# Performance work log

Measured on AMD Instinct MI355X. Metric: run time of the kernel, lower is better.

The kernel has to match this reference:

```python
import jax, jax.numpy as jnp
import numpy as np

N, E, IN, OUT, ED, NT, H = 20000, 640000, 128, 256, 32, 16, 8
GATC = OUT // 2          # 128 per-layer GAT width
C = GATC // H            # 16 per-head dim
GINEC = OUT - GATC       # 128


def setup_inputs() -> dict:
    key = jax.random.key(0)
    ks = jax.random.split(key, 16)
    s = 0.05
    return {
        "x": jax.random.normal(ks[0], (N, IN), jnp.float32),
        "edge_index": jax.random.randint(ks[1], (2, E), 0, N, jnp.int64),
        "edge_attr": jax.random.normal(ks[2], (E, ED), jnp.float32),
        "edge_types": jax.random.randint(ks[3], (E,), 0, NT, jnp.int64),
        "gat_W": jax.random.normal(ks[4], (IN, H * C), jnp.float32) * s,
        "gat_b": jnp.zeros((H * C,), jnp.float32),
        "gat_edge_W": jax.random.normal(ks[5], (ED, H * C), jnp.float32) * s,
        "gat_a_src": jax.random.normal(ks[6], (H, C), jnp.float32) * s,
        "gat_a_dst": jax.random.normal(ks[7], (H, C), jnp.float32) * s,
        "gat_a_edge": jax.random.normal(ks[8], (H, C), jnp.float32) * s,
        "gat_type_emb": jax.random.normal(ks[9], (NT, ED), jnp.float32) * s,
        "gine_type_emb": jax.random.normal(ks[10], (NT, ED), jnp.float32) * s,
        "gine_edge_W": jax.random.normal(ks[11], (ED, IN), jnp.float32) * s,
        "gine_edge_b": jnp.zeros((IN,), jnp.float32),
        "gine_eps": jnp.zeros((1,), jnp.float32),
        "gine_W1": jax.random.normal(ks[12], (IN, GINEC), jnp.float32) * s,
        "gine_b1": jnp.zeros((GINEC,), jnp.float32),
        "gine_W2": jax.random.normal(ks[13], (GINEC, GINEC), jnp.float32) * s,
        "gine_b2": jnp.zeros((GINEC,), jnp.float32),
        "comb_W": jax.random.normal(ks[14], (H * C + GINEC, OUT), jnp.float32) * s,
        "comb_b": jnp.zeros((OUT,), jnp.float32),
        "ln_g": jnp.ones((OUT,), jnp.float32),
        "ln_b": jnp.zeros((OUT,), jnp.float32),
    }


def reference(x, edge_index, edge_attr, edge_types,
              gat_W, gat_b, gat_edge_W, gat_a_src, gat_a_dst, gat_a_edge,
              gat_type_emb, gine_type_emb, gine_edge_W, gine_edge_b, gine_eps,
              gine_W1, gine_b1, gine_W2, gine_b2, comb_W, comb_b, ln_g, ln_b):
    n = x.shape[0]
    h_, c_ = gat_a_src.shape
    src, dst = edge_index[0], edge_index[1]

    # ---- GAT branch (edge-featured multi-head attention) ----
    e = edge_attr + gat_type_emb[edge_types]                      # [E, ED]
    h = (x @ gat_W).reshape(n, h_, c_)                            # [N, H, C]
    ee = (e @ gat_edge_W).reshape(-1, h_, c_)                     # [E, H, C]
    a_s = jnp.einsum('nhc,hc->nh', h, gat_a_src)                  # [N, H]
    a_d = jnp.einsum('nhc,hc->nh', h, gat_a_dst)
    a_e = jnp.einsum('ehc,hc->eh', ee, gat_a_edge)                # [E, H]
    logit = jax.nn.leaky_relu(a_s[src] + a_d[dst] + a_e, 0.2)     # [E, H]
    # segment softmax over incoming edges of each destination node
    mx = jax.ops.segment_max(logit, dst, num_segments=n)
    p = jnp.exp(logit - mx[dst])
    denom = jax.ops.segment_sum(p, dst, num_segments=n)
    alpha = p / (denom[dst] + 1e-16)                              # [E, H]
    msg = alpha[:, :, None] * h[src]                              # [E, H, C]
    gat_out = jax.ops.segment_sum(msg, dst, num_segments=n).reshape(n, h_ * c_) + gat_b

    # ---- GINE branch ----
    ep = (edge_attr + gine_type_emb[edge_types]) @ gine_edge_W + gine_edge_b  # [E, IN]
    agg = jax.ops.segment_sum(jax.nn.relu(x[src] + ep), dst, num_segments=n)
    h2 = (1.0 + gine_eps[0]) * x + agg
    gine_out = jax.nn.relu(h2 @ gine_W1 + gine_b1) @ gine_W2 + gine_b2        # [N, GINEC]

    # ---- fuse: Linear + LayerNorm + ReLU (dropout is identity in eval) ----
    z = jnp.concatenate([gat_out, gine_out], axis=-1) @ comb_W + comb_b       # [N, OUT]
    mu = jnp.mean(z, axis=-1, keepdims=True)
    var = jnp.var(z, axis=-1, keepdims=True)
    z = (z - mu) * jax.lax.rsqrt(var + 1e-5) * ln_g + ln_b
    return jax.nn.relu(z)
```

## Files before the change

### kernel.cpp

```cpp
#include <hip/hip_runtime.h>

#define N_NODES 20000
#define N_EDGES 640000

typedef _Float16 h2v   __attribute__((ext_vector_type(2)));
typedef _Float16 h16x8 __attribute__((ext_vector_type(8)));
typedef float    f32x4v __attribute__((ext_vector_type(4)));
typedef unsigned u32x4v __attribute__((ext_vector_type(4)));

__device__ __forceinline__ unsigned packh2(float a, float b){
    h2v v; v.x = (_Float16)a; v.y = (_Float16)b;
    return __builtin_bit_cast(unsigned, v);
}

__global__ void k0_zero(float4* __restrict__ p, int n4){
    int i = blockIdx.x*blockDim.x + threadIdx.x;
    int stride = gridDim.x*blockDim.x;
    float4 z; z.x=0.f; z.y=0.f; z.z=0.f; z.w=0.f;
    for (; i<n4; i+=stride) p[i] = z;
}

__global__ void kD_detect(const int* __restrict__ eidx_w, const int* __restrict__ ety_w,
                          int* __restrict__ flags){
    int i = blockIdx.x*blockDim.x + threadIdx.x;
    int stride = gridDim.x*blockDim.x;
    int a0 = 0, a1 = 0;
    for (int w = 2*i+1; w < 2*N_EDGES; w += 2*stride) a0 |= eidx_w[w];
    for (int w = 2*i+1; w < N_EDGES;   w += 2*stride) a1 |= ety_w[w];
    if (a0) atomicOr(&flags[0], 1);
    if (a1) atomicOr(&flags[1], 1);
}

__global__ void kN_norm(const int* __restrict__ eidx_w, const int* __restrict__ ety_w,
                        const int* __restrict__ flags,
                        int* __restrict__ dst, int* __restrict__ srcty,
                        int* __restrict__ cnt){
    int i = blockIdx.x*blockDim.x + threadIdx.x;
    int stride = gridDim.x*blockDim.x;
    const bool e32 = (flags[0] != 0);
    const bool t32 = (flags[1] != 0);
    for (int e = i; e < N_EDGES; e += stride){
        int s, d, t;
        if (e32){ s = eidx_w[e];   d = eidx_w[N_EDGES + e]; }
        else    { s = eidx_w[2*e]; d = eidx_w[2*N_EDGES + 2*e]; }
        t = t32 ? ety_w[e] : ety_w[2*e];
        s = min(max(s, 0), N_NODES-1);
        d = min(max(d, 0), N_NODES-1);
        t = min(max(t, 0), 15);
        dst[e] = d; srcty[e] = s | (t << 20);
        atomicAdd(&cnt[d], 1);
    }
}

__global__ __launch_bounds__(1024) void kS_scan(const int* __restrict__ cnt,
                                                int* __restrict__ row_ptr,
                                                int* __restrict__ cursor){
    __shared__ int sW[16];
    __shared__ int sWS[16];
    __shared__ int sbase;
    const int t = threadIdx.x, lane = t & 63, wv = t >> 6;
    if (t==0) sbase = 0;
    __syncthreads();
    for (int base=0; base<N_NODES; base+=4096){
        const int idx0 = base + t*4;
        int v0 = (idx0  <N_NODES) ? cnt[idx0  ] : 0;
        int v1 = (idx0+1<N_NODES) ? cnt[idx0+1] : 0;
        int v2 = (idx0+2<N_NODES) ? cnt[idx0+2] : 0;
        int v3 = (idx0+3<N_NODES) ? cnt[idx0+3] : 0;
        int p1 = v0+v1, p2 = p1+v2, tot = p2+v3;
        int xs = tot;
        #pragma unroll
        for (int off=1; off<64; off<<=1){
            int y = __shfl_up(xs, off, 64);
            if (lane >= off) xs += y;
        }
        if (lane==63) sW[wv] = xs;
        __syncthreads();
        if (t < 16){
            int wvv = sW[t], ws = wvv;
            #pragma unroll
            for (int off=1; off<16; off<<=1){
                int y = __shfl_up(ws, off, 16);
                if ((t&15) >= off) ws += y;
            }
            sWS[t] = ws - wvv;
        }
        __syncthreads();
        int ex = sbase + sWS[wv] + xs - tot;
        if (idx0  <N_NODES){ row_ptr[idx0  ]=ex;    cursor[idx0  ]=ex;    }
        if (idx0+1<N_NODES){ row_ptr[idx0+1]=ex+v0; cursor[idx0+1]=ex+v0; }
        if (idx0+2<N_NODES){ row_ptr[idx0+2]=ex+p1; cursor[idx0+2]=ex+p1; }
        if (idx0+3<N_NODES){ row_ptr[idx0+3]=ex+p2; cursor[idx0+3]=ex+p2; }
        __syncthreads();
        if (t==0) sbase += sWS[15] + sW[15];
        __syncthreads();
    }
    if (t==0) row_ptr[N_NODES] = sbase;
}

__global__ __launch_bounds__(256) void kPre(const float* __restrict__ gat_edge_W,
                                            const float* __restrict__ a_edge,
                                            const float* __restrict__ gat_emb,
                                            const float* __restrict__ gine_emb,
                                            const float* __restrict__ gine_edge_W,
                                            const float* __restrict__ gine_edge_b,
                                            float* __restrict__ Mt, float* __restrict__ ATw,
                                            float* __restrict__ Tw){
    const int t = threadIdx.x;
    if (blockIdx.x < 16){
        if (t < 128){
            const int tyv = blockIdx.x;
            float acc = gine_edge_b[t];
            #pragma unroll
            for (int d=0;d<32;d++) acc += gine_emb[tyv*32+d]*gine_edge_W[d*128+t];
            Tw[tyv*128+t] = acc;
        }
        return;
    }
    __shared__ float sM[32*8];
    const int d = t>>3, hh = t&7;
    float acc = 0.f;
    #pragma unroll
    for (int c=0;c<16;c++) acc += gat_edge_W[d*128 + hh*16 + c]*a_edge[hh*16 + c];
    sM[d*8+hh] = acc; Mt[hh*32 + d] = acc;
    __syncthreads();
    if (t < 128){
        int tyv = t>>3, h2 = t&7;
        float a = 0.f;
        #pragma unroll
        for (int dd=0;dd<32;dd++) a += gat_emb[tyv*32+dd]*sM[dd*8+h2];
        ATw[tyv*8+h2] = a;
    }
}

__global__ __launch_bounds__(128) void k1_node_prep(
    const float* __restrict__ x, const float* __restrict__ gat_W,
    const float* __restrict__ a_src, const float* __restrict__ a_dst,
    unsigned* __restrict__ xhb, float* __restrict__ as_out, float* __restrict__ ad_out)
{
    __shared__ float sX[8][128];
    __shared__ float sH[128];
    const int t = threadIdx.x;
    const int base = blockIdx.x*8;
    const float4* xin = (const float4*)(x + (size_t)base*128);
    float4* sx4 = (float4*)&sX[0][0];
    for (int i=t;i<256;i+=128) sx4[i] = xin[i];
    __syncthreads();
    float acc[8] = {0,0,0,0,0,0,0,0};
    for (int k=0;k<128;k++){
        float w = gat_W[k*128 + t];
        #pragma unroll
        for (int nn=0;nn<8;nn++) acc[nn] += sX[nn][k]*w;
    }
    const float asv = a_src[t], advv = a_dst[t];
    #pragma unroll
    for (int nn=0;nn<8;nn++){
        const int n = base + nn;
        float vs = acc[nn]*asv, vd = acc[nn]*advv;
        #pragma unroll
        for (int off=8; off>=1; off>>=1){ vs += __shfl_xor(vs,off,16); vd += __shfl_xor(vd,off,16); }
        if ((t&15)==0){ as_out[n*8 + (t>>4)] = vs; ad_out[n*8 + (t>>4)] = vd; }
        __syncthreads();
        sH[t] = acc[nn];
        __syncthreads();
        if (t < 64){
            xhb[(size_t)n*128 + t] = packh2(sX[nn][2*t], sX[nn][2*t+1]);
        } else {
            int i = t - 64;
            xhb[(size_t)n*128 + 64 + i] = packh2(sH[2*i], sH[2*i+1]);
        }
    }
}

__global__ __launch_bounds__(256) void kCE_edge(
    const float* __restrict__ eattr,
    const int* __restrict__ dstA, const int* __restrict__ styA,
    const float* __restrict__ a_s, const float* __restrict__ a_d,
    const float* __restrict__ Mt, const float* __restrict__ ATw,
    const float* __restrict__ gine_emb,
    int* __restrict__ cursor,
    unsigned* __restrict__ evb, float* __restrict__ p_s, int* __restrict__ sty_s)
{
    __shared__ float sEv[32][36];
    __shared__ float sMt[8][36];
    __shared__ float sAT[16*8];
    __shared__ int sPos[32];
    const int t = threadIdx.x;
    sMt[t>>5][t&31] = Mt[t];
    if (t < 128) sAT[t] = ATw[t];
    const int et = t>>3, q = t&7;
    for (int base = blockIdx.x*32; base < N_EDGES; base += gridDim.x*32){
        __syncthreads();
        const int e = base + et;
        float4 f = ((const float4*)eattr)[(size_t)e*8 + q];
        *(float4*)&sEv[et][q*4] = f;
        const int d = dstA[e];
        const int sty = styA[e];
        if (q==0) sPos[et] = atomicAdd(&cursor[d], 1);
        __syncthreads();
        const int pos = sPos[et];
        const int srcn = sty & 0xFFFFF;
        const int tyv = ((unsigned)sty)>>20;
        const float4 ge = ((const float4*)gine_emb)[tyv*8 + q];
        ((uint2*)evb)[(size_t)pos*8 + q] =
            make_uint2(packh2(f.x+ge.x, f.y+ge.y), packh2(f.z+ge.z, f.w+ge.w));
        float acc = 0.f;
        #pragma unroll
        for (int m=0;m<8;m++){
            float4 ev4 = *(const float4*)&sEv[et][m*4];
            float4 m4  = *(const float4*)&sMt[q][m*4];
            acc += ev4.x*m4.x + ev4.y*m4.y + ev4.z*m4.z + ev4.w*m4.w;
        }
        float lg = a_s[srcn*8+q] + a_d[d*8+q] + acc + sAT[tyv*8+q];
        lg = (lg>0.f) ? lg : 0.2f*lg;
        p_s[(size_t)pos*8 + q] = __expf(lg);
        if (q==0) sty_s[pos] = sty;
    }
}

template<bool MASK>
__device__ __forceinline__ void gine_block16(
    int pos0, int rem, int m, int g,
    const unsigned* __restrict__ xhb, const unsigned* __restrict__ evb,
    const float* __restrict__ p_s, const int* __restrict__ sty_s,
    const h16x8* aw, const float* bb,
    float* accA, float* accG, float* ps)
{
    const int mc = MASK ? (m < rem ? m : rem - 1) : m;
    u32x4v uu = ((const u32x4v*)evb)[(size_t)(pos0 + mc)*4 + g];
    h16x8 evf = __builtin_bit_cast(h16x8, uu);

    const _Float16* xp[4];
    int ecl[4];
    #pragma unroll
    for (int r=0;r<4;r++){
        const int er = 4*g + r;
        const int ec = MASK ? (er < rem ? er : rem - 1) : er;
        ecl[r] = pos0 + ec;
        const int srcn = sty_s[pos0 + ec] & 0xFFFFF;
        xp[r] = (const _Float16*)(xhb + (size_t)srcn*128) + m;
    }
    #pragma unroll
    for (int hf4=0; hf4<2; hf4++){
        f32x4v pv[4];
        #pragma unroll
        for (int r=0;r<4;r++){
            pv[r] = *(const f32x4v*)(p_s + (size_t)ecl[r]*8 + hf4*4);
            if (MASK && (4*g + r) >= rem) pv[r] = (f32x4v){0.f,0.f,0.f,0.f};
        }
        #pragma unroll
        for (int r=0;r<4;r++){
            ps[hf4*4+0] += pv[r][0]; ps[hf4*4+1] += pv[r][1];
            ps[hf4*4+2] += pv[r][2]; ps[hf4*4+3] += pv[r][3];
        }
        #pragma unroll
        for (int cc=0; cc<4; cc++){
            const int c = hf4*4 + cc;
            f32x4v Dv = { bb[c], bb[c], bb[c], bb[c] };
            Dv = __builtin_amdgcn_mfma_f32_16x16x32_f16(evf, aw[c], Dv, 0, 0, 0);
            #pragma unroll
            for (int r=0;r<4;r++){
                float xf = (float)xp[r][c*16];
                float hf = (float)xp[r][128 + c*16];
                float tmp = fmaxf(xf + Dv[r], 0.f);
                if (MASK && (4*g + r) >= rem) tmp = 0.f;
                accA[c] += tmp;
                accG[c] += pv[r][cc] * hf;
            }
        }
    }
}

__global__ __launch_bounds__(256) void k3_gather(
    const unsigned* __restrict__ xhb, const unsigned* __restrict__ evb,
    const float* __restrict__ p_s, const int* __restrict__ sty_s,
    const int* __restrict__ row_ptr,
    const float* __restrict__ gine_b, const float* __restrict__ gine_W,
    float* __restrict__ agg, float* __restrict__ gacc)
{
    const int t = threadIdx.x;
    const int lane = t & 63;
    const int m = lane & 15;
    const int g = lane >> 4;

    h16x8 aw[8];
    #pragma unroll
    for (int c=0;c<8;c++){
        #pragma unroll
        for (int j=0;j<8;j++)
            aw[c][j] = (_Float16)gine_W[(8*g + j)*128 + c*16 + m];
    }
    float bb[8];
    #pragma unroll
    for (int c=0;c<8;c++) bb[c] = gine_b[c*16 + m];

    const int nwaves = gridDim.x*4;
    for (int d = blockIdx.x*4 + (t>>6); d < N_NODES; d += nwaves){
        const int row = row_ptr[d], end = row_ptr[d+1];
        float accA[8] = {0,0,0,0,0,0,0,0};
        float accG[8] = {0,0,0,0,0,0,0,0};
        float ps[8]   = {0,0,0,0,0,0,0,0};
        const int deg = end - row;
        int pos0 = row;
        const int nfull = deg >> 4;
        for (int b=0;b<nfull;b++, pos0+=16)
            gine_block16<false>(pos0, 16, m, g, xhb, evb, p_s, sty_s, aw, bb, accA, accG, ps);
        const int rem = deg & 15;
        if (rem)
            gine_block16<true>(pos0, rem, m, g, xhb, evb, p_s, sty_s, aw, bb, accA, accG, ps);
        #pragma unroll
        for (int c=0;c<8;c++){
            accA[c] += __shfl_xor(accA[c], 16, 64);
            accA[c] += __shfl_xor(accA[c], 32, 64);
            accG[c] += __shfl_xor(accG[c], 16, 64);
            accG[c] += __shfl_xor(accG[c], 32, 64);
            ps[c]   += __shfl_xor(ps[c],   16, 64);
            ps[c]   += __shfl_xor(ps[c],   32, 64);
        }
        if (g == 0){
            #pragma unroll
            for (int c=0;c<8;c++){
                const float inv = 1.f/(ps[c] + 1e-16f);
                agg [(size_t)d*128 + c*16 + m] = accA[c];
                gacc[(size_t)d*128 + c*16 + m] = accG[c]*inv;
            }
        }
    }
}

#define NPB 8
__global__ __launch_bounds__(256) void k4_final(
    const float* __restrict__ x, const float* __restrict__ agg, const float* __restrict__ gat_acc,
    const float* __restrict__ gat_b, const float* __restrict__ eps_p,
    const float* __restrict__ W1, const float* __restrict__ b1,
    const float* __restrict__ W2, const float* __restrict__ gb2,
    const float* __restrict__ comb_W, const float* __restrict__ comb_b,
    const float* __restrict__ ln_g, const float* __restrict__ ln_b,
    float* __restrict__ out)
{
    __shared__ float sZt[256][NPB];
    __shared__ float sH2[2][128][4];
    __shared__ float sT1[2][128][4];
    __shared__ float sP1[4], sP2[4];
    __shared__ float sMu, sRs;
    const int t = threadIdx.x;
    const int half = t >> 7;
    const int j = t & 127;
    const float epsv = 1.f + eps_p[0];

    {
        float hq[4];
        #pragma unroll
        for (int q=0;q<4;q++){
            const int nn = half*4 + q;
            const int n = blockIdx.x*NPB + nn;
            hq[q] = epsv*x[(size_t)n*128 + j] + agg[(size_t)n*128 + j];
            sZt[j][nn] = gat_acc[(size_t)n*128 + j] + gat_b[j];
        }
        *(float4*)&sH2[half][j][0] = make_float4(hq[0],hq[1],hq[2],hq[3]);
    }
    __syncthreads();
    {
        float acc[4];
        const float b1j = b1[j];
        #pragma unroll
        for (int q=0;q<4;q++) acc[q] = b1j;
        for (int k=0;k<128;k++){
            float w = W1[k*128 + j];
            float4 hv = *(const float4*)&sH2[half][k][0];
            acc[0] += hv.x*w; acc[1] += hv.y*w; acc[2] += hv.z*w; acc[3] += hv.w*w;
        }
        *(float4*)&sT1[half][j][0] = make_float4(fmaxf(acc[0],0.f), fmaxf(acc[1],0.f),
                                                 fmaxf(acc[2],0.f), fmaxf(acc[3],0.f));
    }
    __syncthreads();
    {
        float acc[4];
        const float b2j = gb2[j];
        #pragma unroll
        for (int q=0;q<4;q++) acc[q] = b2j;
        for (int k=0;k<128;k++){
            float w = W2[k*128 + j];
            float4 tv = *(const float4*)&sT1[half][k][0];
            acc[0] += tv.x*w; acc[1] += tv.y*w; acc[2] += tv.z*w; acc[3] += tv.w*w;
        }
        #pragma unroll
        for (int q=0;q<4;q++) sZt[128 + j][half*4 + q] = acc[q];
    }
    __syncthreads();

    float z[NPB];
    const float cb = comb_b[t];
    #pragma unroll
    for (int nn=0;nn<NPB;nn++) z[nn] = cb;
    for (int k=0;k<256;k++){
        float w = comb_W[k*256 + t];
        float4 a = *(const float4*)&sZt[k][0];
        float4 b = *(const float4*)&sZt[k][4];
        z[0] += a.x*w; z[1] += a.y*w; z[2] += a.z*w; z[3] += a.w*w;
        z[4] += b.x*w; z[5] += b.y*w; z[6] += b.z*w; z[7] += b.w*w;
    }

    const float g  = ln_g[t];
    const float bb = ln_b[t];
    for (int nn=0;nn<NPB;nn++){
        const int n = blockIdx.x*NPB + nn;
        float zv = z[nn];
        float s1 = zv, s2 = zv*zv;
        #pragma unroll
        for (int off=32; off>=1; off>>=1){ s1 += __shfl_xor(s1,off,64); s2 += __shfl_xor(s2,off,64); }
        if ((t&63)==0){ sP1[t>>6]=s1; sP2[t>>6]=s2; }
        __syncthreads();
        if (t==0){
            float a1 = sP1[0]+sP1[1]+sP1[2]+sP1[3];
            float a2 = sP2[0]+sP2[1]+sP2[2]+sP2[3];
            float mu = a1*(1.f/256.f);
            float var = a2*(1.f/256.f) - mu*mu;
            sMu = mu; sRs = rsqrtf(var + 1e-5f);
        }
        __syncthreads();
        float r = (zv - sMu)*sRs*g + bb;
        out[(size_t)n*256 + t] = fmaxf(r, 0.f);
        __syncthreads();
    }
}

extern "C" void kernel_launch(void* const* d_in, const int* in_sizes, int n_in,
                              void* d_out, int out_size, void* d_ws, size_t ws_size,
                              hipStream_t stream)
{
    (void)in_sizes; (void)n_in; (void)out_size; (void)ws_size;
    const float* x           = (const float*)d_in[0];
    const int*   eidx_w      = (const int*)  d_in[1];
    const float* eattr       = (const float*)d_in[2];
    const int*   ety_w       = (const int*)  d_in[3];
    const float* gat_W       = (const float*)d_in[4];
    const float* gat_b       = (const float*)d_in[5];
    const float* gat_edge_W  = (const float*)d_in[6];
    const float* a_src       = (const float*)d_in[7];
    const float* a_dst       = (const float*)d_in[8];
    const float* a_edge      = (const float*)d_in[9];
    const float* gat_emb     = (const float*)d_in[10];
    const float* gine_emb    = (const float*)d_in[11];
    const float* gine_edge_W = (const float*)d_in[12];
    const float* gine_edge_b = (const float*)d_in[13];
    const float* gine_eps    = (const float*)d_in[14];
    const float* W1          = (const float*)d_in[15];
    const float* b1          = (const float*)d_in[16];
    const float* W2          = (const float*)d_in[17];
    const float* gb2         = (const float*)d_in[18];
    const float* comb_W      = (const float*)d_in[19];
    const float* comb_b      = (const float*)d_in[20];
    const float* ln_g        = (const float*)d_in[21];
    const float* ln_b        = (const float*)d_in[22];
    float* out = (float*)d_out;

    char* ws = (char*)d_ws;
    size_t off = 0;
    auto alloc = [&](size_t bytes)->void*{ void* p = ws + off; off += (bytes + 255)/256*256; return p; };
    size_t zero_start = off;
    int*      flags  = (int*)     alloc(256);
    int*      cnt    = (int*)     alloc((size_t)N_NODES*4);
    size_t zero_bytes = off - zero_start;
    int*      dstA   = (int*)     alloc((size_t)N_EDGES*4);
    int*      styA   = (int*)     alloc((size_t)N_EDGES*4);
    int*      rowp   = (int*)     alloc((size_t)(N_NODES+1)*4);
    int*      cursor = (int*)     alloc((size_t)N_NODES*4);
    int*      sty_s  = (int*)     alloc((size_t)N_EDGES*4);
    unsigned* evb    = (unsigned*)alloc((size_t)N_EDGES*64);
    float*    p_s    = (float*)   alloc((size_t)N_EDGES*8*4);
    unsigned* xhb    = (unsigned*)alloc((size_t)N_NODES*128*4);
    float*    a_s    = (float*)   alloc((size_t)N_NODES*8*4);
    float*    a_d    = (float*)   alloc((size_t)N_NODES*8*4);
    float*    Mt     = (float*)   alloc(32*8*4);
    float*    ATw    = (float*)   alloc(16*8*4);
    float*    Tw     = (float*)   alloc(16*128*4);
    float*    agg    = (float*)   alloc((size_t)N_NODES*128*4);
    float*    gacc   = (float*)   alloc((size_t)N_NODES*128*4);

    int n4 = (int)(zero_bytes/16);
    k0_zero<<<(n4+255)/256, 256, 0, stream>>>((float4*)(ws + zero_start), n4);
    kD_detect<<<512, 256, 0, stream>>>(eidx_w, ety_w, flags);
    kN_norm<<<1024, 256, 0, stream>>>(eidx_w, ety_w, flags, dstA, styA, cnt);
    kS_scan<<<1, 1024, 0, stream>>>(cnt, rowp, cursor);

    kPre<<<17, 256, 0, stream>>>(gat_edge_W, a_edge, gat_emb, gine_emb,
                                 gine_edge_W, gine_edge_b, Mt, ATw, Tw);
    k1_node_prep<<<N_NODES/8, 128, 0, stream>>>(x, gat_W, a_src, a_dst, xhb, a_s, a_d);

    kCE_edge<<<2500, 256, 0, stream>>>(eattr, dstA, styA, a_s, a_d, Mt, ATw, gine_emb,
                                       cursor, evb, p_s, sty_s);

    k3_gather<<<2500, 256, 0, stream>>>(xhb, evb, p_s, sty_s, rowp,
                                        gine_edge_b, gine_edge_W, agg, gacc);

    k4_final<<<N_NODES/NPB, 256, 0, stream>>>(x, agg, gacc, gat_b, gine_eps,
                                              W1, b1, W2, gb2, comb_W, comb_b,
                                              ln_g, ln_b, out);
}
```

Before: 499.7 us.

## Rewrite final node MLP and combine linear with fp16 MFMA and prepacked weights

Replaces the scalar FP32 GINE MLP, combine linear and LayerNorm kernel with an MFMA 16x16x32 fp16 version that handles 32 nodes per block. A new pre-pass kernel packs W1, W2 and comb_W into fp16 fragment layout. The first GEMM uses a hi/lo fp16 split of the input to keep accuracy. The aim is to cut the FP32 FMA and weight-load cost of the final stage. In exchange, intermediates and weights drop to fp16 precision, and there is one extra small kernel launch.

New measurement: 434.7 us. 13.0% less time.

```diff
diff --git a/kernel.cpp b/kernel.cpp
--- a/kernel.cpp
+++ b/kernel.cpp
@@ -133,6 +133,30 @@
     }
 }
 
+__global__ __launch_bounds__(256) void kW_pack(
+    const float* __restrict__ W1, const float* __restrict__ W2,
+    const float* __restrict__ combW,
+    unsigned* __restrict__ W1p, unsigned* __restrict__ W2p, unsigned* __restrict__ combp)
+{
+    const int tid = blockIdx.x*256 + threadIdx.x;
+    const int chunk = tid >> 6;
+    const int l = tid & 63;
+    const int n = l & 15, g = l >> 4;
+    const float* W; unsigned* P; int NCH, cbase;
+    if (chunk < 32)      { W = W1;    P = W1p;   NCH = 128; cbase = chunk; }
+    else if (chunk < 64) { W = W2;    P = W2p;   NCH = 128; cbase = chunk - 32; }
+    else if (chunk < 192){ W = combW; P = combp; NCH = 256; cbase = chunk - 64; }
+    else return;
+    const int nblocks = NCH/16;
+    const int kstep = cbase / nblocks, nblk = cbase % nblocks;
+    const int k0 = kstep*32 + 8*g, col = nblk*16 + n;
+    unsigned u0 = packh2(W[(size_t)(k0+0)*NCH + col], W[(size_t)(k0+1)*NCH + col]);
+    unsigned u1 = packh2(W[(size_t)(k0+2)*NCH + col], W[(size_t)(k0+3)*NCH + col]);
+    unsigned u2 = packh2(W[(size_t)(k0+4)*NCH + col], W[(size_t)(k0+5)*NCH + col]);
+    unsigned u3 = packh2(W[(size_t)(k0+6)*NCH + col], W[(size_t)(k0+7)*NCH + col]);
+    ((uint4*)P)[(size_t)cbase*64 + l] = make_uint4(u0,u1,u2,u3);
+}
+
 __global__ __launch_bounds__(128) void k1_node_prep(
     const float* __restrict__ x, const float* __restrict__ gat_W,
     const float* __restrict__ a_src, const float* __restrict__ a_dst,
@@ -328,101 +352,184 @@
     }
 }
 
-#define NPB 8
+#define K4N 32
 __global__ __launch_bounds__(256) void k4_final(
-    const float* __restrict__ x, const float* __restrict__ agg, const float* __restrict__ gat_acc,
+    const float* __restrict__ x, const float* __restrict__ agg, const float* __restrict__ gacc,
     const float* __restrict__ gat_b, const float* __restrict__ eps_p,
-    const float* __restrict__ W1, const float* __restrict__ b1,
-    const float* __restrict__ W2, const float* __restrict__ gb2,
-    const float* __restrict__ comb_W, const float* __restrict__ comb_b,
+    const unsigned* __restrict__ W1p, const float* __restrict__ b1,
+    const unsigned* __restrict__ W2p, const float* __restrict__ gb2,
+    const unsigned* __restrict__ combp, const float* __restrict__ comb_b,
     const float* __restrict__ ln_g, const float* __restrict__ ln_b,
     float* __restrict__ out)
 {
-    __shared__ float sZt[256][NPB];
-    __shared__ float sH2[2][128][4];
-    __shared__ float sT1[2][128][4];
-    __shared__ float sP1[4], sP2[4];
-    __shared__ float sMu, sRs;
+    __shared__ _Float16 sHi[K4N][136];
+    __shared__ _Float16 sLo[K4N][136];
+    __shared__ _Float16 sCH[K4N][264];
+    __shared__ float sRed[K4N][8];
+    __shared__ float sMV[K4N][2];
     const int t = threadIdx.x;
-    const int half = t >> 7;
-    const int j = t & 127;
+    const int l = t & 63, wid = t >> 6;
+    const int n = l & 15, g = l >> 4;
     const float epsv = 1.f + eps_p[0];
-
-    {
-        float hq[4];
-        #pragma unroll
-        for (int q=0;q<4;q++){
-            const int nn = half*4 + q;
-            const int n = blockIdx.x*NPB + nn;
-            hq[q] = epsv*x[(size_t)n*128 + j] + agg[(size_t)n*128 + j];
-            sZt[j][nn] = gat_acc[(size_t)n*128 + j] + gat_b[j];
-        }
-        *(float4*)&sH2[half][j][0] = make_float4(hq[0],hq[1],hq[2],hq[3]);
-    }
-    __syncthreads();
-    {
-        float acc[4];
-        const float b1j = b1[j];
-        #pragma unroll
-        for (int q=0;q<4;q++) acc[q] = b1j;
-        for (int k=0;k<128;k++){
-            float w = W1[k*128 + j];
-            float4 hv = *(const float4*)&sH2[half][k][0];
-            acc[0] += hv.x*w; acc[1] += hv.y*w; acc[2] += hv.z*w; acc[3] += hv.w*w;
-        }
-        *(float4*)&sT1[half][j][0] = make_float4(fmaxf(acc[0],0.f), fmaxf(acc[1],0.f),
-                                                 fmaxf(acc[2],0.f), fmaxf(acc[3],0.f));
-    }
-    __syncthreads();
-    {
-        float acc[4];
-        const float b2j = gb2[j];
-        #pragma unroll
-        for (int q=0;q<4;q++) acc[q] = b2j;
-        for (int k=0;k<128;k++){
-            float w = W2[k*128 + j];
-            float4 tv = *(const float4*)&sT1[half][k][0];
-            acc[0] += tv.x*w; acc[1] += tv.y*w; acc[2] += tv.z*w; acc[3] += tv.w*w;
-        }
-        #pragma unroll
-        for (int q=0;q<4;q++) sZt[128 + j][half*4 + q] = acc[q];
-    }
-    __syncthreads();
-
-    float z[NPB];
-    const float cb = comb_b[t];
-    #pragma unroll
-    for (int nn=0;nn<NPB;nn++) z[nn] = cb;
-    for (int k=0;k<256;k++){
-        float w = comb_W[k*256 + t];
-        float4 a = *(const float4*)&sZt[k][0];
-        float4 b = *(const float4*)&sZt[k][4];
-        z[0] += a.x*w; z[1] += a.y*w; z[2] += a.z*w; z[3] += a.w*w;
-        z[4] += b.x*w; z[5] += b.y*w; z[6] += b.z*w; z[7] += b.w*w;
-    }
-
-    const float g  = ln_g[t];
-    const float bb = ln_b[t];
-    for (int nn=0;nn<NPB;nn++){
-        const int n = blockIdx.x*NPB + nn;
-        float zv = z[nn];
-        float s1 = zv, s2 = zv*zv;
-        #pragma unroll
-        for (int off=32; off>=1; off>>=1){ s1 += __shfl_xor(s1,off,64); s2 += __shfl_xor(s2,off,64); }
-        if ((t&63)==0){ sP1[t>>6]=s1; sP2[t>>6]=s2; }
-        __syncthreads();
-        if (t==0){
-            float a1 = sP1[0]+sP1[1]+sP1[2]+sP1[3];
-            float a2 = sP2[0]+sP2[1]+sP2[2]+sP2[3];
-            float mu = a1*(1.f/256.f);
-            float var = a2*(1.f/256.f) - mu*mu;
-            sMu = mu; sRs = rsqrtf(var + 1e-5f);
-        }
-        __syncthreads();
-        float r = (zv - sMu)*sRs*g + bb;
-        out[(size_t)n*256 + t] = fmaxf(r, 0.f);
-        __syncthreads();
-    }
+    const int base = blockIdx.x*K4N;
+
+    for (int i = t; i < K4N*32; i += 256){
+        const int node = i >> 5, c4 = i & 31;
+        float4 xv = ((const float4*)x   )[(size_t)(base+node)*32 + c4];
+        float4 av = ((const float4*)agg )[(size_t)(base+node)*32 + c4];
+        float4 gv = ((const float4*)gacc)[(size_t)(base+node)*32 + c4];
+        float4 bv = ((const float4*)gat_b)[c4];
+        float h0 = epsv*xv.x + av.x, h1 = epsv*xv.y + av.y;
+        float h2_ = epsv*xv.z + av.z, h3 = epsv*xv.w + av.w;
+        _Float16 f0=(_Float16)h0, f1=(_Float16)h1, f2=(_Float16)h2_, f3=(_Float16)h3;
+        h2v p01; p01.x=f0; p01.y=f1;  h2v p23; p23.x=f2; p23.y=f3;
+        *(uint2*)&sHi[node][c4*4] = make_uint2(__builtin_bit_cast(unsigned,p01),
+                                               __builtin_bit_cast(unsigned,p23));
+        h2v q01, q23;
+        q01.x=(_Float16)(h0-(float)f0); q01.y=(_Float16)(h1-(float)f1);
+        q23.x=(_Float16)(h2_-(float)f2); q23.y=(_Float16)(h3-(float)f3);
+        *(uint2*)&sLo[node][c4*4] = make_uint2(__builtin_bit_cast(unsigned,q01),
+                                               __builtin_bit_cast(unsigned,q23));
+        *(uint2*)&sCH[node][c4*4] = make_uint2(packh2(gv.x+bv.x, gv.y+bv.y),
+                                               packh2(gv.z+bv.z, gv.w+bv.w));
+    }
+    __syncthreads();
+
+    f32x4v acc1[2][2];
+    #pragma unroll
+    for (int mt=0;mt<2;mt++)
+        #pragma unroll
+        for (int nt=0;nt<2;nt++){
+            float b = b1[32*wid + 16*nt + n];
+            acc1[mt][nt] = (f32x4v){b,b,b,b};
+        }
+    #pragma unroll
+    for (int ks=0;ks<4;ks++){
+        h16x8 bfr[2];
+        #pragma unroll
+        for (int nt=0;nt<2;nt++){
+            uint4 u = ((const uint4*)W1p)[(size_t)((ks*8 + 2*wid + nt)*64 + l)];
+            bfr[nt] = __builtin_bit_cast(h16x8, u);
+        }
+        #pragma unroll
+        for (int mt=0;mt<2;mt++){
+            const int row = 16*mt + n;
+            h16x8 ahi = *(const h16x8*)&sHi[row][8*g + 32*ks];
+            h16x8 alo = *(const h16x8*)&sLo[row][8*g + 32*ks];
+            #pragma unroll
+            for (int nt=0;nt<2;nt++){
+                acc1[mt][nt] = __builtin_amdgcn_mfma_f32_16x16x32_f16(ahi, bfr[nt], acc1[mt][nt], 0,0,0);
+                acc1[mt][nt] = __builtin_amdgcn_mfma_f32_16x16x32_f16(alo, bfr[nt], acc1[mt][nt], 0,0,0);
+            }
+        }
+    }
+    __syncthreads();
+    #pragma unroll
+    for (int mt=0;mt<2;mt++)
+        #pragma unroll
+        for (int nt=0;nt<2;nt++)
+            #pragma unroll
+            for (int r=0;r<4;r++)
+                sHi[16*mt + 4*g + r][32*wid + 16*nt + n] = (_Float16)fmaxf(acc1[mt][nt][r], 0.f);
+    __syncthreads();
+
+    f32x4v acc2[2][2];
+    #pragma unroll
+    for (int mt=0;mt<2;mt++)
+        #pragma unroll
+        for (int nt=0;nt<2;nt++){
+            float b = gb2[32*wid + 16*nt + n];
+            acc2[mt][nt] = (f32x4v){b,b,b,b};
+        }
+    #pragma unroll
+    for (int ks=0;ks<4;ks++){
+        h16x8 bfr[2];
+        #pragma unroll
+        for (int nt=0;nt<2;nt++){
+            uint4 u = ((const uint4*)W2p)[(size_t)((ks*8 + 2*wid + nt)*64 + l)];
+            bfr[nt] = __builtin_bit_cast(h16x8, u);
+        }
+        #pragma unroll
+        for (int mt=0;mt<2;mt++){
+            h16x8 a = *(const h16x8*)&sHi[16*mt + n][8*g + 32*ks];
+            #pragma unroll
+            for (int nt=0;nt<2;nt++)
+                acc2[mt][nt] = __builtin_amdgcn_mfma_f32_16x16x32_f16(a, bfr[nt], acc2[mt][nt], 0,0,0);
+        }
+    }
+    #pragma unroll
+    for (int mt=0;mt<2;mt++)
+        #pragma unroll
+        for (int nt=0;nt<2;nt++)
+            #pragma unroll
+            for (int r=0;r<4;r++)
+                sCH[16*mt + 4*g + r][128 + 32*wid + 16*nt + n] = (_Float16)acc2[mt][nt][r];
+    __syncthreads();
+
+    f32x4v accC[2][4];
+    #pragma unroll
+    for (int mt=0;mt<2;mt++)
+        #pragma unroll
+        for (int nt=0;nt<4;nt++){
+            float b = comb_b[64*wid + 16*nt + n];
+            accC[mt][nt] = (f32x4v){b,b,b,b};
+        }
+    #pragma unroll
+    for (int ks=0;ks<8;ks++){
+        h16x8 bfr[4];
+        #pragma unroll
+        for (int nt=0;nt<4;nt++){
+            uint4 u = ((const uint4*)combp)[(size_t)((ks*16 + 4*wid + nt)*64 + l)];
+            bfr[nt] = __builtin_bit_cast(h16x8, u);
+        }
+        #pragma unroll
+        for (int mt=0;mt<2;mt++){
+            h16x8 a = *(const h16x8*)&sCH[16*mt + n][8*g + 32*ks];
+            #pragma unroll
+            for (int nt=0;nt<4;nt++)
+                accC[mt][nt] = __builtin_amdgcn_mfma_f32_16x16x32_f16(a, bfr[nt], accC[mt][nt], 0,0,0);
+        }
+    }
+
+    #pragma unroll
+    for (int mt=0;mt<2;mt++)
+        #pragma unroll
+        for (int r=0;r<4;r++){
+            float s1=0.f, s2=0.f;
+            #pragma unroll
+            for (int nt=0;nt<4;nt++){ float z = accC[mt][nt][r]; s1 += z; s2 += z*z; }
+            #pragma unroll
+            for (int off=1; off<16; off<<=1){ s1 += __shfl_xor(s1,off,16); s2 += __shfl_xor(s2,off,16); }
+            if (n==0){
+                sRed[16*mt + 4*g + r][2*wid  ] = s1;
+                sRed[16*mt + 4*g + r][2*wid+1] = s2;
+            }
+        }
+    __syncthreads();
+    if (t < K4N){
+        float a1 = sRed[t][0]+sRed[t][2]+sRed[t][4]+sRed[t][6];
+        float a2 = sRed[t][1]+sRed[t][3]+sRed[t][5]+sRed[t][7];
+        float mu = a1*(1.f/256.f);
+        float var = a2*(1.f/256.f) - mu*mu;
+        sMV[t][0] = mu; sMV[t][1] = rsqrtf(var + 1e-5f);
+    }
+    __syncthreads();
+    float lg[4], lb[4];
+    #pragma unroll
+    for (int nt=0;nt<4;nt++){ int ch = 64*wid + 16*nt + n; lg[nt]=ln_g[ch]; lb[nt]=ln_b[ch]; }
+    #pragma unroll
+    for (int mt=0;mt<2;mt++)
+        #pragma unroll
+        for (int r=0;r<4;r++){
+            const int row = 16*mt + 4*g + r;
+            const float mu = sMV[row][0], rs = sMV[row][1];
+            #pragma unroll
+            for (int nt=0;nt<4;nt++){
+                const int ch = 64*wid + 16*nt + n;
+                float zz = accC[mt][nt][r];
+                out[(size_t)(base+row)*256 + ch] = fmaxf((zz-mu)*rs*lg[nt] + lb[nt], 0.f);
+            }
+        }
 }
 
 extern "C" void kernel_launch(void* const* d_in, const int* in_sizes, int n_in,
@@ -477,6 +584,9 @@
     float*    Tw     = (float*)   alloc(16*128*4);
     float*    agg    = (float*)   alloc((size_t)N_NODES*128*4);
     float*    gacc   = (float*)   alloc((size_t)N_NODES*128*4);
+    unsigned* W1p    = (unsigned*)alloc((size_t)32*1024);
+    unsigned* W2p    = (unsigned*)alloc((size_t)32*1024);
+    unsigned* combp  = (unsigned*)alloc((size_t)128*1024);
 
     int n4 = (int)(zero_bytes/16);
     k0_zero<<<(n4+255)/256, 256, 0, stream>>>((float4*)(ws + zero_start), n4);
@@ -484,6 +594,7 @@
     kN_norm<<<1024, 256, 0, stream>>>(eidx_w, ety_w, flags, dstA, styA, cnt);
     kS_scan<<<1, 1024, 0, stream>>>(cnt, rowp, cursor);
 
+    kW_pack<<<48, 256, 0, stream>>>(W1, W2, comb_W, W1p, W2p, combp);
     kPre<<<17, 256, 0, stream>>>(gat_edge_W, a_edge, gat_emb, gine_emb,
                                  gine_edge_W, gine_edge_b, Mt, ATw, Tw);
     k1_node_prep<<<N_NODES/8, 128, 0, stream>>>(x, gat_W, a_src, a_dst, xhb, a_s, a_d);
@@ -494,7 +605,7 @@
     k3_gather<<<2500, 256, 0, stream>>>(xhb, evb, p_s, sty_s, rowp,
                                         gine_edge_b, gine_edge_W, agg, gacc);
 
-    k4_final<<<N_NODES/NPB, 256, 0, stream>>>(x, agg, gacc, gat_b, gine_eps,
-                                              W1, b1, W2, gb2, comb_W, comb_b,
+    k4_final<<<N_NODES/K4N, 256, 0, stream>>>(x, agg, gacc, gat_b, gine_eps,
+                                              W1p, b1, W2p, gb2, combp, comb_b,
                                               ln_g, ln_b, out);
 }
```
